# Performance work log

Hardware: AMD Instinct MI355X
Metric: run time of the kernel (lower is better)

The kernel has to match this reference:

```python
import jax, jax.numpy as jnp
import numpy as np

D_MODEL, D_QKV, N_HEADS, D_FFN = 2048, 128, 16, 8192
B, L = 2, 2048
EPS = 1e-8
ROPE_THETA = 10000.0


def _rope_cos_sin(seq_len, dim, dtype):
    # interleaved RoPE (rotary_embedding_torch default): pairs (0,1),(2,3),...
    inv_freq = ROPE_THETA ** (-jnp.arange(0, dim, 2, dtype=jnp.float32) / dim)
    ang = jnp.arange(seq_len, dtype=jnp.float32)[:, None] * inv_freq[None, :]  # [L, dim/2]
    return jnp.cos(ang).astype(dtype), jnp.sin(ang).astype(dtype)


def _apply_rope(t, cos, sin):
    # t: [b, h, l, d]; cos/sin: [l, d/2]
    t1, t2 = t[..., 0::2], t[..., 1::2]
    r1 = t1 * cos - t2 * sin
    r2 = t1 * sin + t2 * cos
    return jnp.stack([r1, r2], axis=-1).reshape(t.shape)


def setup_inputs() -> dict:
    key = jax.random.key(0)
    ks = jax.random.split(key, 5)
    d_out = D_QKV * N_HEADS * 3 + D_FFN * 2  # 22528
    return {
        "x": jax.random.normal(ks[0], (B, L, D_MODEL), dtype=jnp.float32),
        "g": jnp.ones((D_MODEL,), dtype=jnp.float32),
        "W_dense": jax.random.normal(ks[1], (d_out, D_MODEL), dtype=jnp.float32) * 0.02,
        "b_dense": jnp.zeros((d_out,), dtype=jnp.float32),
        "W_attn_out": jax.random.normal(ks[2], (D_MODEL, D_QKV * N_HEADS), dtype=jnp.float32) * 0.02,
        "W_ffn_out": jax.random.normal(ks[3], (D_MODEL, D_FFN), dtype=jnp.float32) * 0.02,
    }


def reference(x, g, W_dense, b_dense, W_attn_out, W_ffn_out):
    # RMSNorm (torch.norm variant): x / clamp(||x|| * d^-0.5, eps) * g
    norm = jnp.sqrt(jnp.sum(x * x, axis=-1, keepdims=True)) * (D_MODEL ** -0.5)
    normed = x / jnp.maximum(norm, EPS) * g

    h = jnp.einsum('bld,od->blo', normed, W_dense) + b_dense  # [B, L, 22528]
    dh = D_QKV * N_HEADS
    q, k, v, a, b_gate = jnp.split(h, [dh, 2 * dh, 3 * dh, 3 * dh + D_FFN], axis=-1)

    def to_heads(t):
        return t.reshape(B, L, N_HEADS, D_QKV).transpose(0, 2, 1, 3)  # [b,h,l,d]

    q, k, v = to_heads(q), to_heads(k), to_heads(v)
    cos, sin = _rope_cos_sin(L, D_QKV, x.dtype)
    q = _apply_rope(q, cos, sin)
    k = _apply_rope(k, cos, sin)

    scale = 1.0 / jnp.sqrt(jnp.asarray(D_QKV, dtype=x.dtype))
    scores = jnp.einsum('bhqd,bhkd->bhqk', q, k) * scale
    causal = jnp.tril(jnp.ones((L, L), dtype=bool))
    scores = jnp.where(causal, scores, jnp.asarray(-jnp.inf, dtype=scores.dtype))
    probs = jax.nn.softmax(scores, axis=-1)
    attn = jnp.einsum('bhqk,bhkd->bqhd', probs, v).reshape(B, L, dh)

    attn_out = jnp.einsum('blk,ok->blo', attn, W_attn_out)
    ffn_out = jnp.einsum('blf,of->blo', a * jax.nn.silu(b_gate), W_ffn_out)
    return x + attn_out + ffn_out
```

## Files before the change

kernel.cpp:

```cpp
#include <hip/hip_runtime.h>
#include <hip/hip_bf16.h>
#include <cmath>

typedef __bf16 bf16;
typedef __attribute__((ext_vector_type(8))) __bf16 bf16x8;
typedef __attribute__((ext_vector_type(4))) float f32x4;
typedef unsigned int u32;
typedef unsigned short u16;

#define D_MODEL 2048
#define NH 16
#define DQ 128
#define DH 2048
#define DFFN 8192
#define DOUT 22528
#define BATCH 2
#define SEQ 2048
#define NROWS 4096

__device__ __forceinline__ void gload16(const void* g, void* l) {
    __builtin_amdgcn_global_load_lds((__attribute__((address_space(1))) const void*)g,
                                     (__attribute__((address_space(3))) void*)l, 16, 0, 0);
}

__device__ __forceinline__ float bf2f(u16 u) {
    union { u32 i; float f; } c; c.i = ((u32)u) << 16; return c.f;
}

#define VMW(n)  asm volatile("s_waitcnt vmcnt(" #n ")" ::: "memory")
#define LGK0()  asm volatile("s_waitcnt lgkmcnt(0)" ::: "memory")
#define BARX()  { asm volatile("" ::: "memory"); __builtin_amdgcn_s_barrier(); asm volatile("" ::: "memory"); }

__global__ __launch_bounds__(256) void cvt_f32_bf16(const float* __restrict__ in,
                                                    bf16* __restrict__ out) {
    size_t i = ((size_t)blockIdx.x * 256 + threadIdx.x) * 8;
    float4 a = *(const float4*)(in + i);
    float4 b = *(const float4*)(in + i + 4);
    bf16x8 o;
    o[0]=(bf16)a.x; o[1]=(bf16)a.y; o[2]=(bf16)a.z; o[3]=(bf16)a.w;
    o[4]=(bf16)b.x; o[5]=(bf16)b.y; o[6]=(bf16)b.z; o[7]=(bf16)b.w;
    *(bf16x8*)(out + i) = o;
}

__global__ __launch_bounds__(256) void rmsnorm_k(const float* __restrict__ x,
                                                 const float* __restrict__ g,
                                                 bf16* __restrict__ out) {
    __shared__ float red[4];
    const int row = blockIdx.x;
    const int t = threadIdx.x;
    const float* xr = x + (size_t)row * D_MODEL;
    float4 v0 = *(const float4*)(xr + t*8);
    float4 v1 = *(const float4*)(xr + t*8 + 4);
    float ss = v0.x*v0.x + v0.y*v0.y + v0.z*v0.z + v0.w*v0.w
             + v1.x*v1.x + v1.y*v1.y + v1.z*v1.z + v1.w*v1.w;
    #pragma unroll
    for (int m = 32; m >= 1; m >>= 1) ss += __shfl_xor(ss, m);
    if ((t & 63) == 0) red[t >> 6] = ss;
    __syncthreads();
    float tot = red[0] + red[1] + red[2] + red[3];
    float norm = sqrtf(tot) * 0.022097086912079608f;
    float inv = 1.0f / fmaxf(norm, 1e-8f);
    float4 g0 = *(const float4*)(g + t*8);
    float4 g1 = *(const float4*)(g + t*8 + 4);
    bf16x8 o;
    o[0]=(bf16)(v0.x*inv*g0.x); o[1]=(bf16)(v0.y*inv*g0.y);
    o[2]=(bf16)(v0.z*inv*g0.z); o[3]=(bf16)(v0.w*inv*g0.w);
    o[4]=(bf16)(v1.x*inv*g1.x); o[5]=(bf16)(v1.y*inv*g1.y);
    o[6]=(bf16)(v1.z*inv*g1.z); o[7]=(bf16)(v1.w*inv*g1.w);
    *(bf16x8*)(out + (size_t)row * D_MODEL + t*8) = o;
}

#define SLINE_A(c_, t_) \
    gload16(Asrc + (size_t)((c_)*64)*K + (size_t)(t_)*64, \
            smem + (((t_)&1)<<16) + (c_)*8192 + wid*1024);
#define SLINE_B(c_, t_) \
    gload16(Bsrc + (size_t)((c_)*64)*K + (size_t)(t_)*64, \
            smem + (((t_)&1)<<16) + 32768 + (c_)*8192 + wid*1024);

#define PH_READS_B() \
    _Pragma("unroll") for (int n = 0; n < 4; ++n) { \
        const char* p_ = bb + (wn*64 + n*16 + la) * 128; \
        bfr[n][0] = *(const bf16x8*)(p_ + pg0); \
        bfr[n][1] = *(const bf16x8*)(p_ + pg1); }

#define PH_READS_A(qd_) \
    _Pragma("unroll") for (int mm = 0; mm < 2; ++mm) { \
        const char* p_ = ab + (wm*128 + ((qd_)*2 + mm)*16 + la) * 128; \
        af[mm][0] = *(const bf16x8*)(p_ + pg0); \
        af[mm][1] = *(const bf16x8*)(p_ + pg1); }

#define PH_MFMA(qd_) \
    __builtin_amdgcn_s_setprio(1); \
    _Pragma("unroll") for (int mm = 0; mm < 2; ++mm) \
        _Pragma("unroll") for (int n = 0; n < 4; ++n) { \
            acc[(qd_)*2+mm][n] = __builtin_amdgcn_mfma_f32_16x16x32_bf16(af[mm][0], bfr[n][0], acc[(qd_)*2+mm][n], 0, 0, 0); \
            acc[(qd_)*2+mm][n] = __builtin_amdgcn_mfma_f32_16x16x32_bf16(af[mm][1], bfr[n][1], acc[(qd_)*2+mm][n], 0, 0, 0); } \
    __builtin_amdgcn_s_setprio(0);

template<int MODE>
__global__ __launch_bounds__(512, 2) void gemm256f(
    const bf16* __restrict__ A, const bf16* __restrict__ B,
    int M, int N, int K, int nbx,
    const float* __restrict__ bias, bf16* __restrict__ outb,
    const float* __restrict__ addsrc, float* __restrict__ outf)
{
    __shared__ char smem[131072];
    const int tid = threadIdx.x;
    const int wid = tid >> 6, lane = tid & 63;
    const int la = lane & 15, hi = lane >> 4;
    const int wm = wid >> 2, wn = wid & 3;

    const int nwg = gridDim.x;
    const int cpx = nwg >> 3;
    const int bI = blockIdx.x;
    const int wg = (bI & 7) * cpx + (bI >> 3);
    const int bm = wg / nbx, bn = wg % nbx;
    const size_t m0 = (size_t)bm * 256, n0 = (size_t)bn * 256;

    const int lr = lane >> 3, lg = lane & 7;
    const int sg = lg ^ lr;
    const bf16* Asrc = A + (m0 + wid*8 + lr) * (size_t)K + sg*8;
    const bf16* Bsrc = B + (n0 + wid*8 + lr) * (size_t)K + sg*8;

    const int pg0 = (hi ^ (la & 7)) << 4;
    const int pg1 = ((4 + hi) ^ (la & 7)) << 4;

    f32x4 acc[8][4] = {};
    const int NT = K >> 6;

    SLINE_A(0,0); SLINE_A(2,0);
    SLINE_B(0,0); SLINE_B(1,0);
    SLINE_B(2,0); SLINE_B(3,0);
    SLINE_A(1,0); SLINE_A(3,0);
    VMW(2);
    BARX();

    bf16x8 bfr[4][2];
    bf16x8 af[2][2];

    #pragma unroll 1
    for (int t = 0; t < NT - 1; ++t) {
        const char* ab = smem + ((t & 1) << 16);
        const char* bb = ab + 32768;
        const int nx = t + 1;
        PH_READS_B(); PH_READS_A(0);
        SLINE_A(0,nx); SLINE_A(2,nx);
        BARX(); LGK0(); PH_MFMA(0); BARX();
        PH_READS_A(1);
        SLINE_B(0,nx); SLINE_B(1,nx);
        BARX(); LGK0(); PH_MFMA(1); VMW(4); BARX();
        PH_READS_A(2);
        SLINE_B(2,nx); SLINE_B(3,nx);
        BARX(); LGK0(); PH_MFMA(2); BARX();
        PH_READS_A(3);
        SLINE_A(1,nx); SLINE_A(3,nx);
        BARX(); LGK0(); PH_MFMA(3); VMW(2); BARX();
    }
    {
        const int t = NT - 1;
        const char* ab = smem + ((t & 1) << 16);
        const char* bb = ab + 32768;
        PH_READS_B(); PH_READS_A(0);
        BARX(); LGK0(); PH_MFMA(0); BARX();
        PH_READS_A(1);
        BARX(); LGK0(); PH_MFMA(1); VMW(0); BARX();
        PH_READS_A(2);
        BARX(); LGK0(); PH_MFMA(2); BARX();
        PH_READS_A(3);
        BARX(); LGK0(); PH_MFMA(3); BARX();
    }

    #pragma unroll
    for (int mf = 0; mf < 8; ++mf) {
        const size_t row = m0 + wm*128 + mf*16 + hi*4;
        #pragma unroll
        for (int nf = 0; nf < 4; ++nf) {
            const size_t col = n0 + wn*64 + nf*16 + la;
            if (MODE == 0) {
                const float bv = bias[col];
                #pragma unroll
                for (int r = 0; r < 4; ++r)
                    outb[(row + r) * N + col] = (bf16)(acc[mf][nf][r] + bv);
            } else {
                #pragma unroll
                for (int r = 0; r < 4; ++r) {
                    const size_t off = (row + r) * N + col;
                    outf[off] = addsrc[off] + acc[mf][nf][r];
                }
            }
        }
    }
}

#define OSTAGE_A(st_, c_) { \
    const bf16* s_ = (st_) < 32 ? A1s + (size_t)((c_)*64)*2048 + (size_t)(st_)*64 \
                                : A2s + (size_t)((c_)*64)*8192 + (size_t)((st_)-32)*64; \
    gload16(s_, smem + ((st_)%3)*49152 + (c_)*8192 + wid*1024); }
#define OSTAGE_B(st_, c_) { \
    const bf16* s_ = (st_) < 32 ? B1s + (size_t)((c_)*64)*2048 + (size_t)(st_)*64 \
                                : B2s + (size_t)((c_)*64)*8192 + (size_t)((st_)-32)*64; \
    gload16(s_, smem + ((st_)%3)*49152 + 16384 + (c_)*8192 + wid*1024); }

__global__ __launch_bounds__(512, 2) void gemm_out(
    const bf16* __restrict__ A1, const bf16* __restrict__ B1,
    const bf16* __restrict__ A2, const bf16* __restrict__ B2,
    const float* __restrict__ x, float* __restrict__ outf)
{
    __shared__ char smem[147456];
    const int tid = threadIdx.x;
    const int wid = tid >> 6, lane = tid & 63;
    const int la = lane & 15, hi = lane >> 4;
    const int wm = wid >> 2, wn = wid & 3;

    const int nwg = gridDim.x;
    const int cpx = nwg >> 3;
    const int bI = blockIdx.x;
    const int wg = (bI & 7) * cpx + (bI >> 3);
    const int bm = wg >> 3, bn = wg & 7;
    const size_t m0 = (size_t)bm * 128, n0 = (size_t)bn * 256;

    const int lr = lane >> 3, lg = lane & 7;
    const int sg = lg ^ lr;
    const bf16* A1s = A1 + (m0 + wid*8 + lr) * (size_t)2048 + sg*8;
    const bf16* A2s = A2 + (m0 + wid*8 + lr) * (size_t)8192 + sg*8;
    const bf16* B1s = B1 + (n0 + wid*8 + lr) * (size_t)2048 + sg*8;
    const bf16* B2s = B2 + (n0 + wid*8 + lr) * (size_t)8192 + sg*8;

    const int pg0 = (hi ^ (la & 7)) << 4;
    const int pg1 = ((4 + hi) ^ (la & 7)) << 4;

    f32x4 acc[4][4] = {};
    const int NT = 160;

    OSTAGE_A(0,0); OSTAGE_A(0,1);
    OSTAGE_B(0,0); OSTAGE_B(0,1); OSTAGE_B(0,2); OSTAGE_B(0,3);
    OSTAGE_A(1,0); OSTAGE_A(1,1);
    OSTAGE_B(1,0); OSTAGE_B(1,1); OSTAGE_B(1,2); OSTAGE_B(1,3);
    VMW(6);
    BARX();

    bf16x8 af[4], bfr[4];
    #pragma unroll 1
    for (int t = 0; t < NT; ++t) {
        const char* ab = smem + (t % 3) * 49152;
        const char* bb = ab + 16384;
        const int st = t + 2;
        #pragma unroll
        for (int m = 0; m < 4; ++m) af[m]  = *(const bf16x8*)(ab + (wm*64 + m*16 + la)*128 + pg0);
        #pragma unroll
        for (int n = 0; n < 4; ++n) bfr[n] = *(const bf16x8*)(bb + (wn*64 + n*16 + la)*128 + pg0);
        if (st < NT) { OSTAGE_A(st,0); OSTAGE_A(st,1); OSTAGE_B(st,0); }
        BARX(); LGK0();
        __builtin_amdgcn_s_setprio(1);
        #pragma unroll
        for (int m = 0; m < 4; ++m)
            #pragma unroll
            for (int n = 0; n < 4; ++n)
                acc[m][n] = __builtin_amdgcn_mfma_f32_16x16x32_bf16(af[m], bfr[n], acc[m][n], 0, 0, 0);
        __builtin_amdgcn_s_setprio(0);
        BARX();
        #pragma unroll
        for (int m = 0; m < 4; ++m) af[m]  = *(const bf16x8*)(ab + (wm*64 + m*16 + la)*128 + pg1);
        #pragma unroll
        for (int n = 0; n < 4; ++n) bfr[n] = *(const bf16x8*)(bb + (wn*64 + n*16 + la)*128 + pg1);
        if (st < NT) { OSTAGE_B(st,1); OSTAGE_B(st,2); OSTAGE_B(st,3); }
        if (t < NT - 2) { VMW(6); } else { VMW(0); }
        BARX(); LGK0();
        __builtin_amdgcn_s_setprio(1);
        #pragma unroll
        for (int m = 0; m < 4; ++m)
            #pragma unroll
            for (int n = 0; n < 4; ++n)
                acc[m][n] = __builtin_amdgcn_mfma_f32_16x16x32_bf16(af[m], bfr[n], acc[m][n], 0, 0, 0);
        __builtin_amdgcn_s_setprio(0);
        BARX();
    }

    #pragma unroll
    for (int mf = 0; mf < 4; ++mf) {
        const size_t row = m0 + wm*64 + mf*16 + hi*4;
        #pragma unroll
        for (int nf = 0; nf < 4; ++nf) {
            const size_t col = n0 + wn*64 + nf*16 + la;
            #pragma unroll
            for (int r = 0; r < 4; ++r) {
                const size_t off = (row + r) * (size_t)DH + col;
                outf[off] = x[off] + acc[mf][nf][r];
            }
        }
    }
}

__global__ __launch_bounds__(256) void rope_table(float* __restrict__ ctab,
                                                  float* __restrict__ stab) {
    int idx = blockIdx.x * 256 + threadIdx.x;
    int l = idx >> 6, i = idx & 63;
    float inv = powf(10000.0f, -(float)i / 64.0f);
    float ang = (float)l * inv;
    float s, c;
    sincosf(ang, &s, &c);
    ctab[idx] = c; stab[idx] = s;
}

__device__ __forceinline__ u32 rope_pair(u32 u, float c, float s) {
    float t1 = bf2f((u16)(u & 0xffff));
    float t2 = bf2f((u16)(u >> 16));
    float r1 = t1 * c - t2 * s;
    float r2 = t1 * s + t2 * c;
    bf16 b1 = (bf16)r1, b2 = (bf16)r2;
    return (u32)__builtin_bit_cast(u16, b1) | ((u32)__builtin_bit_cast(u16, b2) << 16);
}

__global__ __launch_bounds__(256) void rope_qk(const bf16* __restrict__ h,
                                               const float* __restrict__ ctab,
                                               const float* __restrict__ stab,
                                               bf16* __restrict__ qb, bf16* __restrict__ kb) {
    int idx = blockIdx.x * 256 + threadIdx.x;
    int i  = idx & 63;
    int hh = (idx >> 6) & 15;
    int l  = (idx >> 10) & 2047;
    int b  = idx >> 21;
    size_t hrow = (size_t)(b * SEQ + l) * DOUT;
    float c = ctab[l*64 + i], s = stab[l*64 + i];
    u32 uq = *(const u32*)(h + hrow + hh*DQ + 2*i);
    u32 uk = *(const u32*)(h + hrow + DH + hh*DQ + 2*i);
    size_t orow = ((size_t)(b*NH + hh) * SEQ + l) * DQ + 2*i;
    *(u32*)(qb + orow) = rope_pair(uq, c, s);
    *(u32*)(kb + orow) = rope_pair(uk, c, s);
}

__global__ __launch_bounds__(256) void v_transpose(const bf16* __restrict__ h,
                                                   bf16* __restrict__ vt) {
    __shared__ u32 lds[64][68];
    const int lt = blockIdx.x, bh = blockIdx.y;
    const int b = bh >> 4, hh = bh & 15;
    const int t = threadIdx.x;
    const bf16* src = h + (size_t)(b * SEQ + lt * 64) * DOUT + 2*DH + hh * DQ;
    #pragma unroll
    for (int i = 0; i < 4; ++i) {
        int j = i*256 + t;
        int l = j >> 4, ch = j & 15;
        uint4 v = *(const uint4*)(src + (size_t)l * DOUT + ch*8);
        *(uint4*)&lds[l][ch*4] = v;
    }
    __syncthreads();
    bf16* dst = vt + (size_t)bh * DQ * SEQ + lt * 64;
    #pragma unroll
    for (int i = 0; i < 4; ++i) {
        int j = i*256 + t;
        int d = j >> 3, lc = j & 7;
        u32 out[4];
        #pragma unroll
        for (int m = 0; m < 4; ++m) {
            u32 a0 = lds[lc*8 + 2*m][d >> 1];
            u32 a1 = lds[lc*8 + 2*m + 1][d >> 1];
            u16 s0 = (d & 1) ? (u16)(a0 >> 16) : (u16)(a0 & 0xffff);
            u16 s1 = (d & 1) ? (u16)(a1 >> 16) : (u16)(a1 & 0xffff);
            out[m] = (u32)s0 | ((u32)s1 << 16);
        }
        *(uint4*)(dst + (size_t)d * SEQ + lc*8) = *(uint4*)out;
    }
}

__global__ __launch_bounds__(256) void silu_k(const bf16* __restrict__ h,
                                              bf16* __restrict__ ag) {
    size_t idx = ((size_t)blockIdx.x * 256 + threadIdx.x) * 8;
    int r = (int)(idx >> 13);
    int f = (int)(idx & 8191);
    const bf16* hr = h + (size_t)r * DOUT + 3*DH;
    bf16x8 va = *(const bf16x8*)(hr + f);
    bf16x8 vb = *(const bf16x8*)(hr + DFFN + f);
    bf16x8 o;
    #pragma unroll
    for (int j = 0; j < 8; ++j) {
        float a = (float)va[j];
        float b = (float)vb[j];
        float sil = b / (1.0f + __expf(-b));
        o[j] = (bf16)(a * sil);
    }
    *(bf16x8*)(ag + idx) = o;
}

__global__ __launch_bounds__(256) void attn_fa(const bf16* __restrict__ Q,
                                               const bf16* __restrict__ Kb,
                                               const bf16* __restrict__ Vt,
                                               bf16* __restrict__ O) {
    __shared__ bf16 Ks[64][128];
    __shared__ bf16 Vts[128][64];
    __shared__ bf16 Ps[4][16][64];
    const int qt = blockIdx.x, bh = blockIdx.y;
    const int b = bh >> 4, hh = bh & 15;
    const int tid = threadIdx.x, wid = tid >> 6, lane = tid & 63;
    const int la = lane & 15, hi = lane >> 4;
    const bf16* Qp = Q + (size_t)bh * SEQ * DQ;
    const bf16* Kp = Kb + (size_t)bh * SEQ * DQ;
    const bf16* Vp = Vt + (size_t)bh * DQ * SEQ;
    const int q0w = qt * 64 + wid * 16;

    bf16x8 qf[4];
    #pragma unroll
    for (int s = 0; s < 4; ++s)
        qf[s] = *(const bf16x8*)(Qp + (size_t)(q0w + la) * DQ + s*32 + hi*8);

    f32x4 acc_o[8] = {};
    float m_run[4] = {-1e30f, -1e30f, -1e30f, -1e30f};
    float l_run[4] = {0.f, 0.f, 0.f, 0.f};
    const float scale = 0.08838834764831845f;

    const int nk = qt + 1;
    for (int kt = 0; kt < nk; ++kt) {
        const int k0 = kt * 64;
        __syncthreads();
        #pragma unroll
        for (int i = 0; i < 4; ++i) {
            int j = i*256 + tid;
            int kr = j >> 4, jg = j & 15;
            gload16(Kp + (size_t)(k0 + kr) * DQ + ((jg ^ (kr & 7)) << 3),
                    (char*)Ks + i*4096 + wid*1024);
            int d = j >> 3, vg = j & 7;
            gload16(Vp + (size_t)d * SEQ + k0 + ((vg ^ (d & 7)) << 3),
                    (char*)Vts + i*4096 + wid*1024);
        }
        __syncthreads();

        f32x4 sacc[4] = {};
        __builtin_amdgcn_s_setprio(1);
        #pragma unroll
        for (int g = 0; g < 4; ++g) {
            const int krow = g*16 + la;
            #pragma unroll
            for (int s = 0; s < 4; ++s) {
                bf16x8 kf = *(const bf16x8*)((const char*)Ks + krow*256 + (((s*4 + hi) ^ (la & 7)) << 4));
                sacc[g] = __builtin_amdgcn_mfma_f32_16x16x32_bf16(qf[s], kf, sacc[g], 0, 0, 0);
            }
        }
        __builtin_amdgcn_s_setprio(0);

        float mnew[4];
        #pragma unroll
        for (int r = 0; r < 4; ++r) mnew[r] = m_run[r];
        #pragma unroll
        for (int g = 0; g < 4; ++g)
            #pragma unroll
            for (int r = 0; r < 4; ++r) {
                float sv = sacc[g][r] * scale;
                int qi = q0w + hi*4 + r;
                int ki = k0 + g*16 + la;
                sv = (ki <= qi) ? sv : -1e30f;
                sacc[g][r] = sv;
                mnew[r] = fmaxf(mnew[r], sv);
            }
        #pragma unroll
        for (int r = 0; r < 4; ++r) {
            float v = mnew[r];
            v = fmaxf(v, __shfl_xor(v, 1));
            v = fmaxf(v, __shfl_xor(v, 2));
            v = fmaxf(v, __shfl_xor(v, 4));
            v = fmaxf(v, __shfl_xor(v, 8));
            mnew[r] = v;
        }
        float resc[4], lsum[4];
        #pragma unroll
        for (int r = 0; r < 4; ++r) {
            resc[r] = __expf(m_run[r] - mnew[r]);
            m_run[r] = mnew[r];
            lsum[r] = 0.f;
        }
        #pragma unroll
        for (int g = 0; g < 4; ++g)
            #pragma unroll
            for (int r = 0; r < 4; ++r) {
                float p = __expf(sacc[g][r] - mnew[r]);
                sacc[g][r] = p;
                lsum[r] += p;
            }
        #pragma unroll
        for (int r = 0; r < 4; ++r) {
            float v = lsum[r];
            v += __shfl_xor(v, 1); v += __shfl_xor(v, 2);
            v += __shfl_xor(v, 4); v += __shfl_xor(v, 8);
            l_run[r] = l_run[r] * resc[r] + v;
        }
        #pragma unroll
        for (int g = 0; g < 4; ++g)
            #pragma unroll
            for (int r = 0; r < 4; ++r) {
                int prow = hi*4 + r;
                int pcol = (g*16 + la) ^ ((prow & 7) << 3);
                Ps[wid][prow][pcol] = (bf16)sacc[g][r];
            }
        #pragma unroll
        for (int n = 0; n < 8; ++n)
            #pragma unroll
            for (int r = 0; r < 4; ++r) acc_o[n][r] *= resc[r];
        __builtin_amdgcn_s_setprio(1);
        #pragma unroll
        for (int kk = 0; kk < 2; ++kk) {
            bf16x8 pf = *(const bf16x8*)((const char*)&Ps[wid][0][0] + la*128 +
                                         (((kk*32 + hi*8) ^ ((la & 7) << 3)) << 1));
            #pragma unroll
            for (int n = 0; n < 8; ++n) {
                const int vrow = n*16 + la;
                bf16x8 vf = *(const bf16x8*)((const char*)Vts + vrow*128 + (((kk*4 + hi) ^ (la & 7)) << 4));
                acc_o[n] = __builtin_amdgcn_mfma_f32_16x16x32_bf16(pf, vf, acc_o[n], 0, 0, 0);
            }
        }
        __builtin_amdgcn_s_setprio(0);
    }

    bf16* Op = O + (size_t)b * SEQ * DH + (size_t)hh * DQ;
    #pragma unroll
    for (int r = 0; r < 4; ++r) {
        int qi = q0w + hi*4 + r;
        float invl = 1.0f / l_run[r];
        #pragma unroll
        for (int n = 0; n < 8; ++n)
            Op[(size_t)qi * DH + n*16 + la] = (bf16)(acc_o[n][r] * invl);
    }
}

extern "C" void kernel_launch(void* const* d_in, const int* in_sizes, int n_in,
                              void* d_out, int out_size, void* d_ws, size_t ws_size,
                              hipStream_t stream) {
    const float* x       = (const float*)d_in[0];
    const float* g       = (const float*)d_in[1];
    const float* W_dense = (const float*)d_in[2];
    const float* b_dense = (const float*)d_in[3];
    const float* W_attn  = (const float*)d_in[4];
    const float* W_ffn   = (const float*)d_in[5];
    float* out = (float*)d_out;

    char* ws = (char*)d_ws;
    bf16* normed  = (bf16*)(ws + 0);
    bf16* Wd_b    = (bf16*)(ws + 16777216);
    bf16* Wa_b    = (bf16*)(ws + 109051904);
    bf16* Wf_b    = (bf16*)(ws + 117440512);
    bf16* h_b     = (bf16*)(ws + 150994944);
    bf16* ag_b    = (bf16*)(ws + 335544320);
    float* ctab   = (float*)(ws + 402653184);
    float* stab   = (float*)(ws + 403177472);
    bf16* q_b  = (bf16*)(ws + 16777216);
    bf16* k_b  = (bf16*)(ws + 16777216 + 16777216);
    bf16* vt_b = (bf16*)(ws + 16777216 + 33554432);
    bf16* attn_b = normed;

    cvt_f32_bf16<<<46137344/2048, 256, 0, stream>>>(W_dense, Wd_b);
    cvt_f32_bf16<<<4194304/2048, 256, 0, stream>>>(W_attn, Wa_b);
    cvt_f32_bf16<<<16777216/2048, 256, 0, stream>>>(W_ffn, Wf_b);
    rmsnorm_k<<<NROWS, 256, 0, stream>>>(x, g, normed);
    {
        dim3 grid((NROWS/256) * (DOUT/256));
        gemm256f<0><<<grid, 512, 0, stream>>>(normed, Wd_b, NROWS, DOUT, D_MODEL,
                                              DOUT/256, b_dense, h_b, nullptr, nullptr);
    }
    rope_table<<<SEQ*64/256, 256, 0, stream>>>(ctab, stab);
    rope_qk<<<4194304/256, 256, 0, stream>>>(h_b, ctab, stab, q_b, k_b);
    {
        dim3 grid(SEQ/64, BATCH*NH);
        v_transpose<<<grid, 256, 0, stream>>>(h_b, vt_b);
    }
    silu_k<<<(size_t)NROWS*DFFN/8/256, 256, 0, stream>>>(h_b, ag_b);
    {
        dim3 grid(SEQ/64, BATCH*NH);
        attn_fa<<<grid, 256, 0, stream>>>(q_b, k_b, vt_b, attn_b);
    }
    gemm_out<<<256, 512, 0, stream>>>(attn_b, Wa_b, ag_b, Wf_b, x, out);
}
```

Measured before the change: 845.9 us.

## Fuse SiLU gating into dense GEMM epilogue via interleaved weight rows

Reorders the W_dense rows during bf16 conversion so that a and gate columns are interleaved in 16-wide groups, letting the dense GEMM epilogue compute a*silu(b) directly and write the FFN activation. The separate silu kernel goes away, and so does writing and re-reading the 4096x16384 bf16 a/gate half of h. Only the QKV part (6144 columns) is now stored in h. It also swaps the block index mapping to be M-fastest and hardcodes K. The cost is a strided gather in the weight conversion and a heavier epilogue.

```diff
diff --git a/kernel.cpp b/kernel.cpp
--- a/kernel.cpp
+++ b/kernel.cpp
@@ -14,6 +14,7 @@
 #define DH 2048
 #define DFFN 8192
 #define DOUT 22528
+#define HQKV 6144
 #define BATCH 2
 #define SEQ 2048
 #define NROWS 4096
@@ -36,6 +37,28 @@
     size_t i = ((size_t)blockIdx.x * 256 + threadIdx.x) * 8;
     float4 a = *(const float4*)(in + i);
     float4 b = *(const float4*)(in + i + 4);
+    bf16x8 o;
+    o[0]=(bf16)a.x; o[1]=(bf16)a.y; o[2]=(bf16)a.z; o[3]=(bf16)a.w;
+    o[4]=(bf16)b.x; o[5]=(bf16)b.y; o[6]=(bf16)b.z; o[7]=(bf16)b.w;
+    *(bf16x8*)(out + i) = o;
+}
+
+__global__ __launch_bounds__(256) void cvt_wd(const float* __restrict__ in,
+                                              bf16* __restrict__ out) {
+    size_t i = ((size_t)blockIdx.x * 256 + threadIdx.x) * 8;
+    int nr = (int)(i >> 11);
+    int c  = (int)(i & 2047);
+    int orig;
+    if (nr < HQKV) orig = nr;
+    else {
+        int gg = nr - HQKV;
+        int blk = gg >> 4;
+        int f = ((blk >> 1) << 4) + (gg & 15);
+        orig = (blk & 1) ? (3*DH + DFFN + f) : (3*DH + f);
+    }
+    const float* src = in + (size_t)orig * 2048 + c;
+    float4 a = *(const float4*)src;
+    float4 b = *(const float4*)(src + 4);
     bf16x8 o;
     o[0]=(bf16)a.x; o[1]=(bf16)a.y; o[2]=(bf16)a.z; o[3]=(bf16)a.w;
     o[4]=(bf16)b.x; o[5]=(bf16)b.y; o[6]=(bf16)b.z; o[7]=(bf16)b.w;
@@ -71,10 +94,10 @@
 }
 
 #define SLINE_A(c_, t_) \
-    gload16(Asrc + (size_t)((c_)*64)*K + (size_t)(t_)*64, \
+    gload16(Asrc + (size_t)((c_)*64)*2048 + (size_t)(t_)*64, \
             smem + (((t_)&1)<<16) + (c_)*8192 + wid*1024);
 #define SLINE_B(c_, t_) \
-    gload16(Bsrc + (size_t)((c_)*64)*K + (size_t)(t_)*64, \
+    gload16(Bsrc + (size_t)((c_)*64)*2048 + (size_t)(t_)*64, \
             smem + (((t_)&1)<<16) + 32768 + (c_)*8192 + wid*1024);
 
 #define PH_READS_B() \
@@ -97,12 +120,10 @@
             acc[(qd_)*2+mm][n] = __builtin_amdgcn_mfma_f32_16x16x32_bf16(af[mm][1], bfr[n][1], acc[(qd_)*2+mm][n], 0, 0, 0); } \
     __builtin_amdgcn_s_setprio(0);
 
-template<int MODE>
-__global__ __launch_bounds__(512, 2) void gemm256f(
+__global__ __launch_bounds__(512, 2) void gemm_dense(
     const bf16* __restrict__ A, const bf16* __restrict__ B,
-    int M, int N, int K, int nbx,
-    const float* __restrict__ bias, bf16* __restrict__ outb,
-    const float* __restrict__ addsrc, float* __restrict__ outf)
+    const float* __restrict__ bias, bf16* __restrict__ h6,
+    bf16* __restrict__ ag)
 {
     __shared__ char smem[131072];
     const int tid = threadIdx.x;
@@ -114,19 +135,19 @@
     const int cpx = nwg >> 3;
     const int bI = blockIdx.x;
     const int wg = (bI & 7) * cpx + (bI >> 3);
-    const int bm = wg / nbx, bn = wg % nbx;
+    const int bn = wg >> 4, bm = wg & 15;
     const size_t m0 = (size_t)bm * 256, n0 = (size_t)bn * 256;
 
     const int lr = lane >> 3, lg = lane & 7;
     const int sg = lg ^ lr;
-    const bf16* Asrc = A + (m0 + wid*8 + lr) * (size_t)K + sg*8;
-    const bf16* Bsrc = B + (n0 + wid*8 + lr) * (size_t)K + sg*8;
+    const bf16* Asrc = A + (m0 + wid*8 + lr) * (size_t)2048 + sg*8;
+    const bf16* Bsrc = B + (n0 + wid*8 + lr) * (size_t)2048 + sg*8;
 
     const int pg0 = (hi ^ (la & 7)) << 4;
     const int pg1 = ((4 + hi) ^ (la & 7)) << 4;
 
     f32x4 acc[8][4] = {};
-    const int NT = K >> 6;
+    const int NT = 32;
 
     SLINE_A(0,0); SLINE_A(2,0);
     SLINE_B(0,0); SLINE_B(1,0);
@@ -170,22 +191,36 @@
         BARX(); LGK0(); PH_MFMA(3); BARX();
     }
 
-    #pragma unroll
-    for (int mf = 0; mf < 8; ++mf) {
-        const size_t row = m0 + wm*128 + mf*16 + hi*4;
-        #pragma unroll
-        for (int nf = 0; nf < 4; ++nf) {
-            const size_t col = n0 + wn*64 + nf*16 + la;
-            if (MODE == 0) {
+    if (n0 < HQKV) {
+        #pragma unroll
+        for (int mf = 0; mf < 8; ++mf) {
+            const size_t row = m0 + wm*128 + mf*16 + hi*4;
+            #pragma unroll
+            for (int nf = 0; nf < 4; ++nf) {
+                const size_t col = n0 + wn*64 + nf*16 + la;
                 const float bv = bias[col];
                 #pragma unroll
                 for (int r = 0; r < 4; ++r)
-                    outb[(row + r) * N + col] = (bf16)(acc[mf][nf][r] + bv);
-            } else {
+                    h6[(row + r) * HQKV + col] = (bf16)(acc[mf][nf][r] + bv);
+            }
+        }
+    } else {
+        #pragma unroll
+        for (int mf = 0; mf < 8; ++mf) {
+            const size_t row = m0 + wm*128 + mf*16 + hi*4;
+            #pragma unroll
+            for (int np = 0; np < 4; np += 2) {
+                const int col_a = (int)n0 + wn*64 + np*16 + la;
+                const int gg = col_a - HQKV;
+                const int f = ((gg >> 5) << 4) + (gg & 15);
+                const float ba = bias[3*DH + f];
+                const float bb2 = bias[3*DH + DFFN + f];
                 #pragma unroll
                 for (int r = 0; r < 4; ++r) {
-                    const size_t off = (row + r) * N + col;
-                    outf[off] = addsrc[off] + acc[mf][nf][r];
+                    float a = acc[mf][np][r] + ba;
+                    float b = acc[mf][np+1][r] + bb2;
+                    float sil = b / (1.0f + __expf(-b));
+                    ag[(row + r) * (size_t)DFFN + f] = (bf16)(a * sil);
                 }
             }
         }
@@ -320,7 +355,7 @@
     int hh = (idx >> 6) & 15;
     int l  = (idx >> 10) & 2047;
     int b  = idx >> 21;
-    size_t hrow = (size_t)(b * SEQ + l) * DOUT;
+    size_t hrow = (size_t)(b * SEQ + l) * HQKV;
     float c = ctab[l*64 + i], s = stab[l*64 + i];
     u32 uq = *(const u32*)(h + hrow + hh*DQ + 2*i);
     u32 uk = *(const u32*)(h + hrow + DH + hh*DQ + 2*i);
@@ -335,12 +370,12 @@
     const int lt = blockIdx.x, bh = blockIdx.y;
     const int b = bh >> 4, hh = bh & 15;
     const int t = threadIdx.x;
-    const bf16* src = h + (size_t)(b * SEQ + lt * 64) * DOUT + 2*DH + hh * DQ;
+    const bf16* src = h + (size_t)(b * SEQ + lt * 64) * HQKV + 2*DH + hh * DQ;
     #pragma unroll
     for (int i = 0; i < 4; ++i) {
         int j = i*256 + t;
         int l = j >> 4, ch = j & 15;
-        uint4 v = *(const uint4*)(src + (size_t)l * DOUT + ch*8);
+        uint4 v = *(const uint4*)(src + (size_t)l * HQKV + ch*8);
         *(uint4*)&lds[l][ch*4] = v;
     }
     __syncthreads();
@@ -360,25 +395,6 @@
         }
         *(uint4*)(dst + (size_t)d * SEQ + lc*8) = *(uint4*)out;
     }
-}
-
-__global__ __launch_bounds__(256) void silu_k(const bf16* __restrict__ h,
-                                              bf16* __restrict__ ag) {
-    size_t idx = ((size_t)blockIdx.x * 256 + threadIdx.x) * 8;
-    int r = (int)(idx >> 13);
-    int f = (int)(idx & 8191);
-    const bf16* hr = h + (size_t)r * DOUT + 3*DH;
-    bf16x8 va = *(const bf16x8*)(hr + f);
-    bf16x8 vb = *(const bf16x8*)(hr + DFFN + f);
-    bf16x8 o;
-    #pragma unroll
-    for (int j = 0; j < 8; ++j) {
-        float a = (float)va[j];
-        float b = (float)vb[j];
-        float sil = b / (1.0f + __expf(-b));
-        o[j] = (bf16)(a * sil);
-    }
-    *(bf16x8*)(ag + idx) = o;
 }
 
 __global__ __launch_bounds__(256) void attn_fa(const bf16* __restrict__ Q,
@@ -544,14 +560,13 @@
     bf16* vt_b = (bf16*)(ws + 16777216 + 33554432);
     bf16* attn_b = normed;
 
-    cvt_f32_bf16<<<46137344/2048, 256, 0, stream>>>(W_dense, Wd_b);
+    cvt_wd<<<46137344/2048, 256, 0, stream>>>(W_dense, Wd_b);
     cvt_f32_bf16<<<4194304/2048, 256, 0, stream>>>(W_attn, Wa_b);
     cvt_f32_bf16<<<16777216/2048, 256, 0, stream>>>(W_ffn, Wf_b);
     rmsnorm_k<<<NROWS, 256, 0, stream>>>(x, g, normed);
     {
         dim3 grid((NROWS/256) * (DOUT/256));
-        gemm256f<0><<<grid, 512, 0, stream>>>(normed, Wd_b, NROWS, DOUT, D_MODEL,
-                                              DOUT/256, b_dense, h_b, nullptr, nullptr);
+        gemm_dense<<<grid, 512, 0, stream>>>(normed, Wd_b, b_dense, h_b, ag_b);
     }
     rope_table<<<SEQ*64/256, 256, 0, stream>>>(ctab, stab);
     rope_qk<<<4194304/256, 256, 0, stream>>>(h_b, ctab, stab, q_b, k_b);
@@ -559,7 +574,6 @@
         dim3 grid(SEQ/64, BATCH*NH);
         v_transpose<<<grid, 256, 0, stream>>>(h_b, vt_b);
     }
-    silu_k<<<(size_t)NROWS*DFFN/8/256, 256, 0, stream>>>(h_b, ag_b);
     {
         dim3 grid(SEQ/64, BATCH*NH);
         attn_fa<<<grid, 256, 0, stream>>>(q_b, k_b, vt_b, attn_b);
```

After: 819.9 us. 1.03x faster.
